# Kernel tuning notes

Hardware: AMD Instinct MI355X
Metric: run time of the kernel (lower is better)

The kernel has to match this reference:

```python
import jax, jax.numpy as jnp
import numpy as np

IN_CH, OUT_CH, K, N = 32, 64, 7, 64  # input_channels, output_channels, kernel_size, input_size


def _pad_kernel(kernel):
    # Replicates OpticalConv2dNew.process_inputs/__pad for K < N:
    # symmetric pad by (N-K)//2, then (0,1,0,1) if size still off by one.
    p = (N - K) // 2
    extra = 1 if (K + 2 * p) != N else 0
    return jnp.pad(kernel, ((0, 0), (0, 0), (p, p + extra), (p, p + extra)))


def _opt_conv(img, ker):
    # Ideal 4f optical convolution (FFT-based, circular): |fftshift(ifft2(fft2(ifftshift(x)) * fft2(ifftshift(h))))|
    ax = (-2, -1)
    F = jnp.fft.fft2(jnp.fft.ifftshift(img, axes=ax))      # (B,1,in,N,N) complex
    G = jnp.fft.fft2(jnp.fft.ifftshift(ker, axes=ax))      # (1,out,in,N,N) complex
    out = jnp.fft.fftshift(jnp.fft.ifft2(F * G), axes=ax)  # (B,out,in,N,N)
    return jnp.abs(out)


def setup_inputs() -> dict:
    key = jax.random.key(0)
    k1, k2 = jax.random.split(key)
    B = 8
    inputs = {
        "input": jax.random.normal(k1, (B, IN_CH, N, N), dtype=jnp.float32),
        # kaiming-uniform-like init for the learned kernel parameter
        "kernel": jax.random.uniform(k2, (OUT_CH, IN_CH, K, K), dtype=jnp.float32,
                                     minval=-1.0, maxval=1.0) * float(np.sqrt(6.0 / (IN_CH * K * K))),
    }
    return inputs


def reference(input, kernel):
    ker = _pad_kernel(kernel)                 # (out,in,N,N)
    img = input[:, None, :, :, :]             # (B,1,in,N,N) — broadcast instead of repeat/reshape
    ker = ker[None, :, :, :, :]               # (1,out,in,N,N)
    out = _opt_conv(img, ker)                 # (B,out,in,N,N) float32 (abs of complex)
    return jnp.sum(out, axis=2)               # sum over input channels -> (B,out,N,N)
```

## Files before the change

### kernel.cpp

```cpp
#include <hip/hip_runtime.h>

typedef __attribute__((ext_vector_type(8))) short short8;
typedef __attribute__((ext_vector_type(4))) float f32x4;

namespace {

__device__ __forceinline__ unsigned short f2bf(float f) {
    unsigned int u = __float_as_uint(f);
    u += 0x7fffu + ((u >> 16) & 1u);
    return (unsigned short)(u >> 16);
}

__global__ void prep_B(const float* __restrict__ ker, uint4* __restrict__ B2) {
    int t  = blockIdx.x * 256 + threadIdx.x;
    int a  = t & 7;
    int oc = (t >> 3) & 63;
    int ic = t >> 9;
    unsigned int d[4] = {0u, 0u, 0u, 0u};
    if (a < 7) {
        const float* row = ker + ((oc * 32 + ic) * 49) + (6 - a) * 7;
        float v[8];
#pragma unroll
        for (int q = 0; q < 7; ++q) v[q] = row[6 - q];
        v[7] = 0.0f;
#pragma unroll
        for (int j = 0; j < 4; ++j)
            d[j] = (unsigned int)f2bf(v[2 * j]) | ((unsigned int)f2bf(v[2 * j + 1]) << 16);
    }
    int ot = oc >> 4, n = oc & 15, kt = a >> 2, g = a & 3;
    B2[(ic * 8 + ot * 2 + kt) * 64 + g * 16 + n] = make_uint4(d[0], d[1], d[2], d[3]);
}

__global__ __launch_bounds__(1024, 4) void conv_mfma(
    const float* __restrict__ img,
    const uint4* __restrict__ B2,
    float* __restrict__ out)
{
    __shared__ unsigned int H[18576];

    const int bid  = blockIdx.x;
    const int yp   = bid & 31;
    const int b    = bid >> 5;
    const int y0   = yp * 2;
    const int tid  = threadIdx.x;
    const int lane = tid & 63;
    const int w    = tid >> 6;
    const int xh   = w & 1;
    const int icg  = w >> 1;
    const int n    = lane & 15;
    const int g    = lane >> 4;

    const float* base = img + (size_t)b * 32 * 4096;

    if (tid < 144) H[18432 + tid] = 0u;

    float v[16];
#pragma unroll
    for (int j = 0; j < 16; ++j) {
        const int pl  = 2 * w + (j >> 3);
        const int row = (y0 - 2 + (j & 7)) & 63;
        v[j] = base[pl * 4096 + row * 64 + lane];
    }
#pragma unroll
    for (int j = 0; j < 16; ++j) {
        const int pl = 2 * w + (j >> 3);
        const int r  = j & 7;
        const unsigned int h  = f2bf(v[j]);
        const unsigned int hn = (unsigned int)__shfl((int)h, (lane + 1) & 63);
        const unsigned int dw = h | (hn << 16);
        const int idx = pl * 576 + r * 72;
        H[idx + lane + 2] = dw;
        if (lane >= 62) H[idx + lane - 62] = dw;
        if (lane <= 5)  H[idx + lane + 66] = dw;
    }
    __syncthreads();

    f32x4 acc[4][4];
#pragma unroll
    for (int nt = 0; nt < 4; ++nt)
#pragma unroll
        for (int ot = 0; ot < 4; ++ot) acc[nt][ot] = (f32x4){0.f, 0.f, 0.f, 0.f};

#pragma unroll 1
    for (int ici = 0; ici < 4; ++ici) {
        const int ic = icg * 4 + ici;
        uint4 bf[8];
#pragma unroll
        for (int q = 0; q < 8; ++q)
            bf[q] = B2[(ic * 8 + q) * 64 + lane];

#pragma unroll
        for (int nt = 0; nt < 4; ++nt) {
            const int b0 = ic * 576 + ((nt >> 1) + g) * 72 + 32 * xh + 16 * (nt & 1) + n;
            const int b1 = b0 + 288;
            uint4 i0 = make_uint4(H[b0], H[b0 + 2], H[b0 + 4], H[b0 + 6]);
            uint4 i1 = make_uint4(H[b1], H[b1 + 2], H[b1 + 4], H[b1 + 6]);
            short8 f0 = __builtin_bit_cast(short8, i0);
            short8 f1 = __builtin_bit_cast(short8, i1);
#pragma unroll
            for (int ot = 0; ot < 4; ++ot) {
                f32x4 d = (f32x4){0.f, 0.f, 0.f, 0.f};
                d = __builtin_amdgcn_mfma_f32_16x16x32_bf16(
                        __builtin_bit_cast(short8, bf[2 * ot]),     f0, d, 0, 0, 0);
                d = __builtin_amdgcn_mfma_f32_16x16x32_bf16(
                        __builtin_bit_cast(short8, bf[2 * ot + 1]), f1, d, 0, 0, 0);
#pragma unroll
                for (int i = 0; i < 4; ++i)
                    acc[nt][ot][i] += __builtin_fabsf(d[i]);
            }
        }
    }

    float* P = (float*)H;
    __syncthreads();

#pragma unroll
    for (int ph = 0; ph < 2; ++ph) {
        if (icg >= 4) {
            const int rb = ((icg - 4) * 2 + xh) * 2048;
#pragma unroll
            for (int nh = 0; nh < 2; ++nh) {
                const int nt = 2 * ph + nh;
                float* q = P + rb + (nh * 4 + 0) * 256 + lane * 4;
#pragma unroll
                for (int ot = 0; ot < 4; ++ot)
#pragma unroll
                    for (int i = 0; i < 4; ++i)
                        P[rb + (nh * 4 + ot) * 256 + lane * 4 + i] = acc[nt][ot][i];
                (void)q;
            }
        }
        __syncthreads();
        if (icg < 4) {
            const int rb = (icg * 2 + xh) * 2048;
#pragma unroll
            for (int nh = 0; nh < 2; ++nh) {
                const int nt = 2 * ph + nh;
#pragma unroll
                for (int ot = 0; ot < 4; ++ot)
#pragma unroll
                    for (int i = 0; i < 4; ++i)
                        acc[nt][ot][i] += P[rb + (nh * 4 + ot) * 256 + lane * 4 + i];
            }
        }
        __syncthreads();
    }
    if (icg == 2 || icg == 3) {
        const int rb = ((icg - 2) * 2 + xh) * 4096;
#pragma unroll
        for (int nt = 0; nt < 4; ++nt)
#pragma unroll
            for (int ot = 0; ot < 4; ++ot)
#pragma unroll
                for (int i = 0; i < 4; ++i)
                    P[rb + (nt * 4 + ot) * 256 + lane * 4 + i] = acc[nt][ot][i];
    }
    __syncthreads();
    if (icg == 0 || icg == 1) {
        const int rb = (icg * 2 + xh) * 4096;
#pragma unroll
        for (int nt = 0; nt < 4; ++nt)
#pragma unroll
            for (int ot = 0; ot < 4; ++ot)
#pragma unroll
                for (int i = 0; i < 4; ++i)
                    acc[nt][ot][i] += P[rb + (nt * 4 + ot) * 256 + lane * 4 + i];
    }
    __syncthreads();
    if (icg == 1) {
        const int rb = xh * 4096;
#pragma unroll
        for (int nt = 0; nt < 4; ++nt)
#pragma unroll
            for (int ot = 0; ot < 4; ++ot)
#pragma unroll
                for (int i = 0; i < 4; ++i)
                    P[rb + (nt * 4 + ot) * 256 + lane * 4 + i] = acc[nt][ot][i];
    }
    __syncthreads();
    if (icg == 0) {
        const int rb = xh * 4096;
        float* o = out + (size_t)b * 64 * 4096;
#pragma unroll
        for (int nt = 0; nt < 4; ++nt) {
            const int y  = y0 + (nt >> 1);
            const int x0 = 32 * xh + 16 * (nt & 1);
#pragma unroll
            for (int ot = 0; ot < 4; ++ot)
#pragma unroll
                for (int i = 0; i < 4; ++i) {
                    const int oc = 16 * ot + 4 * g + i;
                    o[(size_t)oc * 4096 + y * 64 + x0 + n] =
                        acc[nt][ot][i] + P[rb + (nt * 4 + ot) * 256 + lane * 4 + i];
                }
        }
    }
}

}

extern "C" void kernel_launch(void* const* d_in, const int* in_sizes, int n_in,
                              void* d_out, int out_size, void* d_ws, size_t ws_size,
                              hipStream_t stream) {
    const float* img = (const float*)d_in[0];
    const float* ker = (const float*)d_in[1];
    float* out = (float*)d_out;
    uint4* B2 = (uint4*)d_ws;

    prep_B<<<dim3(64), dim3(256), 0, stream>>>(ker, B2);
    conv_mfma<<<dim3(256), dim3(1024), 0, stream>>>(img, B2, out);
}
```

Measured before the change: 74.33 us.

## Split blocks across x-halves and simplify cross-wave channel reduction

The grid now uses 512 blocks of 512 threads, each covering half the image width. Every wave owns four input channels for the whole half-tile, so each wave loads and converts only the columns it needs into a narrower LDS layout, and the barrier after staging is dropped. The multi-stage tree reduction of per-wave accumulators is replaced by one LDS pass per row tile, with all waves summing across the eight channel groups and writing outputs directly. This gives more blocks per GPU and shorter reduction chains, at the cost of more barriers inside the output loop and some redundant halo loads.

```diff
diff --git a/kernel.cpp b/kernel.cpp
--- a/kernel.cpp
+++ b/kernel.cpp
@@ -27,53 +27,47 @@
         for (int j = 0; j < 4; ++j)
             d[j] = (unsigned int)f2bf(v[2 * j]) | ((unsigned int)f2bf(v[2 * j + 1]) << 16);
     }
-    int ot = oc >> 4, n = oc & 15, kt = a >> 2, g = a & 3;
-    B2[(ic * 8 + ot * 2 + kt) * 64 + g * 16 + n] = make_uint4(d[0], d[1], d[2], d[3]);
+    int ot = oc >> 4, nn = oc & 15, kt = a >> 2, gg = a & 3;
+    B2[(ic * 8 + ot * 2 + kt) * 64 + gg * 16 + nn] = make_uint4(d[0], d[1], d[2], d[3]);
 }
 
-__global__ __launch_bounds__(1024, 4) void conv_mfma(
+__global__ __launch_bounds__(512, 4) void conv_mfma(
     const float* __restrict__ img,
     const uint4* __restrict__ B2,
     float* __restrict__ out)
 {
-    __shared__ unsigned int H[18576];
+    __shared__ unsigned int H[10240];
+    __shared__ float P[8192];
 
     const int bid  = blockIdx.x;
-    const int yp   = bid & 31;
-    const int b    = bid >> 5;
+    const int xh   = bid & 1;
+    const int yp   = (bid >> 1) & 31;
+    const int b    = bid >> 6;
     const int y0   = yp * 2;
     const int tid  = threadIdx.x;
     const int lane = tid & 63;
     const int w    = tid >> 6;
-    const int xh   = w & 1;
-    const int icg  = w >> 1;
     const int n    = lane & 15;
     const int g    = lane >> 4;
 
     const float* base = img + (size_t)b * 32 * 4096;
 
-    if (tid < 144) H[18432 + tid] = 0u;
-
-    float v[16];
+    const int colg = (32 * xh + lane - 2) & 63;
+    float v[32];
 #pragma unroll
-    for (int j = 0; j < 16; ++j) {
-        const int pl  = 2 * w + (j >> 3);
+    for (int j = 0; j < 32; ++j) {
+        const int ic  = w * 4 + (j >> 3);
         const int row = (y0 - 2 + (j & 7)) & 63;
-        v[j] = base[pl * 4096 + row * 64 + lane];
+        v[j] = base[ic * 4096 + row * 64 + colg];
     }
 #pragma unroll
-    for (int j = 0; j < 16; ++j) {
-        const int pl = 2 * w + (j >> 3);
+    for (int j = 0; j < 32; ++j) {
+        const int ic = w * 4 + (j >> 3);
         const int r  = j & 7;
         const unsigned int h  = f2bf(v[j]);
         const unsigned int hn = (unsigned int)__shfl((int)h, (lane + 1) & 63);
-        const unsigned int dw = h | (hn << 16);
-        const int idx = pl * 576 + r * 72;
-        H[idx + lane + 2] = dw;
-        if (lane >= 62) H[idx + lane - 62] = dw;
-        if (lane <= 5)  H[idx + lane + 66] = dw;
+        if (lane < 38) H[ic * 320 + r * 40 + lane] = h | (hn << 16);
     }
-    __syncthreads();
 
     f32x4 acc[4][4];
 #pragma unroll
@@ -83,7 +77,7 @@
 
 #pragma unroll 1
     for (int ici = 0; ici < 4; ++ici) {
-        const int ic = icg * 4 + ici;
+        const int ic = w * 4 + ici;
         uint4 bf[8];
 #pragma unroll
         for (int q = 0; q < 8; ++q)
@@ -91,10 +85,15 @@
 
 #pragma unroll
         for (int nt = 0; nt < 4; ++nt) {
-            const int b0 = ic * 576 + ((nt >> 1) + g) * 72 + 32 * xh + 16 * (nt & 1) + n;
-            const int b1 = b0 + 288;
-            uint4 i0 = make_uint4(H[b0], H[b0 + 2], H[b0 + 4], H[b0 + 6]);
-            uint4 i1 = make_uint4(H[b1], H[b1 + 2], H[b1 + 4], H[b1 + 6]);
+            const int ry = nt >> 1;
+            const int s0 = 16 * (nt & 1) + n;
+            const int r0 = ry + g;
+            int r1 = r0 + 4;
+            if (r1 > 7) r1 = 7;
+            const int d0 = ic * 320 + r0 * 40 + s0;
+            const int d1 = ic * 320 + r1 * 40 + s0;
+            uint4 i0 = make_uint4(H[d0], H[d0 + 2], H[d0 + 4], H[d0 + 6]);
+            uint4 i1 = make_uint4(H[d1], H[d1 + 2], H[d1 + 4], H[d1 + 6]);
             short8 f0 = __builtin_bit_cast(short8, i0);
             short8 f1 = __builtin_bit_cast(short8, i1);
 #pragma unroll
@@ -111,89 +110,35 @@
         }
     }
 
-    float* P = (float*)H;
-    __syncthreads();
-
+    const int ot_r = w >> 1;
+    const int ih   = w & 1;
+    float* o = out + (size_t)b * 64 * 4096;
 #pragma unroll
-    for (int ph = 0; ph < 2; ++ph) {
-        if (icg >= 4) {
-            const int rb = ((icg - 4) * 2 + xh) * 2048;
+    for (int nt = 0; nt < 4; ++nt) {
 #pragma unroll
-            for (int nh = 0; nh < 2; ++nh) {
-                const int nt = 2 * ph + nh;
-                float* q = P + rb + (nh * 4 + 0) * 256 + lane * 4;
-#pragma unroll
-                for (int ot = 0; ot < 4; ++ot)
-#pragma unroll
-                    for (int i = 0; i < 4; ++i)
-                        P[rb + (nh * 4 + ot) * 256 + lane * 4 + i] = acc[nt][ot][i];
-                (void)q;
-            }
+        for (int ot = 0; ot < 4; ++ot) {
+            const int idx = (w * 4 + ot) * 128 + lane * 2;
+            P[idx]            = acc[nt][ot][0];
+            P[idx + 1]        = acc[nt][ot][1];
+            P[4096 + idx]     = acc[nt][ot][2];
+            P[4096 + idx + 1] = acc[nt][ot][3];
         }
         __syncthreads();
-        if (icg < 4) {
-            const int rb = (icg * 2 + xh) * 2048;
+        {
+            float s0 = 0.f, s1 = 0.f;
 #pragma unroll
-            for (int nh = 0; nh < 2; ++nh) {
-                const int nt = 2 * ph + nh;
-#pragma unroll
-                for (int ot = 0; ot < 4; ++ot)
-#pragma unroll
-                    for (int i = 0; i < 4; ++i)
-                        acc[nt][ot][i] += P[rb + (nh * 4 + ot) * 256 + lane * 4 + i];
+            for (int icg = 0; icg < 8; ++icg) {
+                const int idx = ih * 4096 + (icg * 4 + ot_r) * 128 + lane * 2;
+                s0 += P[idx];
+                s1 += P[idx + 1];
             }
+            const int y   = y0 + (nt >> 1);
+            const int xg  = 32 * xh + 16 * (nt & 1) + n;
+            const int oc0 = 16 * ot_r + 4 * g + 2 * ih;
+            o[(size_t)oc0 * 4096 + y * 64 + xg]       = s0;
+            o[(size_t)(oc0 + 1) * 4096 + y * 64 + xg] = s1;
         }
         __syncthreads();
-    }
-    if (icg == 2 || icg == 3) {
-        const int rb = ((icg - 2) * 2 + xh) * 4096;
-#pragma unroll
-        for (int nt = 0; nt < 4; ++nt)
-#pragma unroll
-            for (int ot = 0; ot < 4; ++ot)
-#pragma unroll
-                for (int i = 0; i < 4; ++i)
-                    P[rb + (nt * 4 + ot) * 256 + lane * 4 + i] = acc[nt][ot][i];
-    }
-    __syncthreads();
-    if (icg == 0 || icg == 1) {
-        const int rb = (icg * 2 + xh) * 4096;
-#pragma unroll
-        for (int nt = 0; nt < 4; ++nt)
-#pragma unroll
-            for (int ot = 0; ot < 4; ++ot)
-#pragma unroll
-                for (int i = 0; i < 4; ++i)
-                    acc[nt][ot][i] += P[rb + (nt * 4 + ot) * 256 + lane * 4 + i];
-    }
-    __syncthreads();
-    if (icg == 1) {
-        const int rb = xh * 4096;
-#pragma unroll
-        for (int nt = 0; nt < 4; ++nt)
-#pragma unroll
-            for (int ot = 0; ot < 4; ++ot)
-#pragma unroll
-                for (int i = 0; i < 4; ++i)
-                    P[rb + (nt * 4 + ot) * 256 + lane * 4 + i] = acc[nt][ot][i];
-    }
-    __syncthreads();
-    if (icg == 0) {
-        const int rb = xh * 4096;
-        float* o = out + (size_t)b * 64 * 4096;
-#pragma unroll
-        for (int nt = 0; nt < 4; ++nt) {
-            const int y  = y0 + (nt >> 1);
-            const int x0 = 32 * xh + 16 * (nt & 1);
-#pragma unroll
-            for (int ot = 0; ot < 4; ++ot)
-#pragma unroll
-                for (int i = 0; i < 4; ++i) {
-                    const int oc = 16 * ot + 4 * g + i;
-                    o[(size_t)oc * 4096 + y * 64 + x0 + n] =
-                        acc[nt][ot][i] + P[rb + (nt * 4 + ot) * 256 + lane * 4 + i];
-                }
-        }
     }
 }
 
@@ -208,5 +153,5 @@
     uint4* B2 = (uint4*)d_ws;
 
     prep_B<<<dim3(64), dim3(256), 0, stream>>>(ker, B2);
-    conv_mfma<<<dim3(256), dim3(1024), 0, stream>>>(img, B2, out);
+    conv_mfma<<<dim3(512), dim3(512), 0, stream>>>(img, B2, out);
 }
```

Measured after the change: 74.84 us. No clear change (+0.7%).
